# Performance work log

Measured on AMD Instinct MI355X. Metric: run time of the kernel, lower is better.

The kernel has to match this reference:

```python
import jax, jax.numpy as jnp
import numpy as np

jax.config.update("jax_enable_x64", True)  # hash math needs int64 (prime * coord > 2^31)

LEVEL = 16
MOD_T = 2 ** 16
FDIM = 3
_PRIMES = (1, 2654435761, 805459861)  # first feature_dim primes from the module


def _grid_sizes():
    # mirrors torch float32 computation: b = exp((log(n_max)-log(n_min))/(level-1))
    n_min = np.float32(4.0)
    n_max = np.float32(256.0)
    b = np.float32(np.exp((np.log(n_max) - np.log(n_min)) / np.float32(LEVEL - 1)))
    return [int(n_min * b ** i) for i in range(LEVEL)]


def setup_inputs() -> dict:
    key = jax.random.key(0)
    k1, k2 = jax.random.split(key)
    images = jax.random.uniform(k1, (16, 3, 256, 256), dtype=jnp.float32)
    hash_table = (jax.random.uniform(k2, (LEVEL, MOD_T, FDIM), dtype=jnp.float32)
                  * 0.0002 - 0.0001)
    return {"images": images, "hash_table": hash_table}


def reference(images, hash_table):
    b, c, h, w = images.shape
    primes = jnp.array(_PRIMES[:FDIM], dtype=jnp.int64)
    neg_inf = jnp.array(-jnp.inf, dtype=images.dtype)
    outs = []
    for lvl, grid in enumerate(_grid_sizes()):
        kh, kw = h // grid, w // grid
        # max_pool2d(images*grid, kernel=(kh,kw), stride=(kh,kw))
        pooled = jax.lax.reduce_window(
            images * grid, neg_inf, jax.lax.max,
            window_dimensions=(1, 1, kh, kw),
            window_strides=(1, 1, kh, kw),
            padding="VALID")                     # [B, F, gh, gw]
        idx = pooled.astype(jnp.int64) * primes[None, :, None, None]
        g = idx[:, 0]
        for i in range(1, FDIM):
            g = g ^ idx[:, i]
        g = g % MOD_T                             # [B, gh, gw]
        f = hash_table[lvl][g]                    # gather -> [B, gh, gw, F]
        f = jnp.transpose(f, (0, 3, 1, 2))        # [B, F, gh, gw]
        # F.interpolate(..., mode='bilinear') == half-pixel, align_corners=False
        f = jax.image.resize(f, (b, FDIM, h, w), method="bilinear")
        outs.append(f)
    return jnp.concatenate(outs, axis=1)          # [B, level*F, H, W]
```

## Files before the change

### kernel.cpp

```cpp
#include <hip/hip_runtime.h>
#include <stdint.h>
#include <math.h>


#define NLVL 16
#define NB   16

__constant__ int   c_P[NLVL]   = {4,5,6,9,12,15,21,28,36,51,64,85,128,256,256,256};
__constant__ float c_G[NLVL]   = {4.f,5.f,6.f,9.f,12.f,15.f,21.f,27.f,36.f,48.f,63.f,84.f,111.f,147.f,194.f,255.f};
__constant__ int   c_CUM[14]   = {0,16,41,77,158,302,527,968,1752,3048,5649,9745,16970,33354};

#define CELLS_PB   33354
#define CELLS_TOT  (CELLS_PB*NB)
#define MWS_FLOATS (CELLS_TOT*3)
#define POOL_BLOCKS (NB*32)
#define DIR_BLOCKS  1024
#define TILE_BLOCKS (13*16*16)
#define K2_BLOCKS   (DIR_BLOCKS + TILE_BLOCKS)

__device__ __forceinline__ uint32_t hash3(float m0, float m1, float m2, float g) {
    uint32_t v0 = (uint32_t)(int)(m0 * g);
    uint32_t v1 = (uint32_t)(int)(m1 * g);
    uint32_t v2 = (uint32_t)(int)(m2 * g);
    return (v0 ^ (v1 * 2654435761u) ^ (v2 * 805459861u)) & 0xFFFFu;
}

__global__ __launch_bounds__(256) void pool_single(const float* __restrict__ img,
                                                   unsigned int* __restrict__ mws)
{
    static constexpr int K_P[13]   = {4,5,6,9,12,15,21,28,36,51,64,85,128};
    static constexpr int K_KH[13]  = {64,51,42,28,21,17,12,9,7,5,4,3,2};
    static constexpr int K_CUM[13] = {0,16,41,77,158,302,527,968,1752,3048,5649,9745,16970};

    __shared__ float simg[3][8][256];
    __shared__ float colbuf[3][256];

    int b    = blockIdx.x >> 5;
    int band = blockIdx.x & 31;
    int y0   = band * 8;

    const float* base = img + (size_t)b * 196608 + (size_t)y0 * 256;
    for (int t = threadIdx.x; t < 1536; t += 256) {
        int ch = t >> 9;
        int r  = t & 511;
        float4 v = *(const float4*)(base + (size_t)ch * 65536 + r * 4);
        int row = r >> 6, c4 = (r & 63) << 2;
        simg[ch][row][c4 + 0] = v.x;
        simg[ch][row][c4 + 1] = v.y;
        simg[ch][row][c4 + 2] = v.z;
        simg[ch][row][c4 + 3] = v.w;
    }
    __syncthreads();

    int x = threadIdx.x;
#pragma unroll
    for (int lvl = 0; lvl < 13; ++lvl) {
        const int kh = K_KH[lvl], P = K_P[lvl];
        int nr0 = y0 / kh;
        int nr1 = (y0 + 7) / kh; if (nr1 > P - 1) nr1 = P - 1;
        for (int cr = nr0; cr <= nr1; ++cr) {
            int rlo = cr * kh;      if (rlo < y0) rlo = y0;
            int rhi = cr * kh + kh; if (rhi > y0 + 8) rhi = y0 + 8;
            float p0 = -INFINITY, p1 = -INFINITY, p2 = -INFINITY;
            for (int r = rlo; r < rhi; ++r) {
                int rr = r - y0;
                p0 = fmaxf(p0, simg[0][rr][x]);
                p1 = fmaxf(p1, simg[1][rr][x]);
                p2 = fmaxf(p2, simg[2][rr][x]);
            }
            colbuf[0][x] = p0; colbuf[1][x] = p1; colbuf[2][x] = p2;
            __syncthreads();
            if (x < P) {
                float q0 = -INFINITY, q1 = -INFINITY, q2 = -INFINITY;
                for (int c = x * kh; c < x * kh + kh; ++c) {
                    q0 = fmaxf(q0, colbuf[0][c]);
                    q1 = fmaxf(q1, colbuf[1][c]);
                    q2 = fmaxf(q2, colbuf[2][c]);
                }
                int idx = K_CUM[lvl] * NB + b * P * P + cr * P + x;
                atomicMax(&mws[idx],                 __float_as_uint(q0));
                atomicMax(&mws[idx + CELLS_TOT],     __float_as_uint(q1));
                atomicMax(&mws[idx + 2 * CELLS_TOT], __float_as_uint(q2));
            }
            __syncthreads();
        }
    }
}

__global__ __launch_bounds__(256) void render(const float* __restrict__ img,
                                              const float* __restrict__ tab,
                                              const float* __restrict__ mws,
                                              float* __restrict__ out)
{
    __shared__ float4 s[34 * 34];
    if (blockIdx.x < DIR_BLOCKS) {
        int t = blockIdx.x * 256 + threadIdx.x;
        int b = t >> 14;
        int pix0 = (t & 16383) << 2;
        const float* p = img + (size_t)b * 196608 + pix0;
        float4 i0 = *(const float4*)p;
        float4 i1 = *(const float4*)(p + 65536);
        float4 i2 = *(const float4*)(p + 131072);
#pragma unroll
        for (int lvl = 13; lvl < 16; ++lvl) {
            float g = c_G[lvl];
            const float* T = tab + (size_t)lvl * 196608;
            uint32_t g0 = hash3(i0.x, i1.x, i2.x, g);
            uint32_t g1 = hash3(i0.y, i1.y, i2.y, g);
            uint32_t g2 = hash3(i0.z, i1.z, i2.z, g);
            uint32_t g3 = hash3(i0.w, i1.w, i2.w, g);
            float3 f0 = *(const float3*)(T + g0 * 3);
            float3 f1 = *(const float3*)(T + g1 * 3);
            float3 f2 = *(const float3*)(T + g2 * 3);
            float3 f3 = *(const float3*)(T + g3 * 3);
            float4 o0, o1, o2;
            o0.x = f0.x; o1.x = f0.y; o2.x = f0.z;
            o0.y = f1.x; o1.y = f1.y; o2.y = f1.z;
            o0.z = f2.x; o1.z = f2.y; o2.z = f2.z;
            o0.w = f3.x; o1.w = f3.y; o2.w = f3.z;
            float* ob = out + ((size_t)b * 48 + 3 * lvl) * 65536 + pix0;
            *(float4*)ob            = o0;
            *(float4*)(ob + 65536)  = o1;
            *(float4*)(ob + 131072) = o2;
        }
        return;
    }

    int blk   = blockIdx.x - DIR_BLOCKS;
    int tile  = blk & 15;
    int plane = blk >> 4;
    int lvl   = plane >> 4;
    int b     = plane & 15;
    int P     = c_P[lvl];
    int yt0   = (tile >> 2) * 64;
    int xt0   = (tile & 3) * 64;

    int nlo  = ((2 * yt0 + 1) * P - 256) >> 9;
    int r_lo = nlo < 0 ? 0 : (nlo > P - 1 ? P - 1 : nlo);
    int nhi  = (((2 * (yt0 + 63) + 1) * P - 256) >> 9) + 1;
    int r_hi = nhi < 0 ? 0 : (nhi > P - 1 ? P - 1 : nhi);
    int mlo  = ((2 * xt0 + 1) * P - 256) >> 9;
    int c_lo = mlo < 0 ? 0 : (mlo > P - 1 ? P - 1 : mlo);
    int mhi  = (((2 * (xt0 + 63) + 1) * P - 256) >> 9) + 1;
    int c_hi = mhi < 0 ? 0 : (mhi > P - 1 ? P - 1 : mhi);
    int span_y = r_hi - r_lo + 1;
    int span_x = c_hi - c_lo + 1;

    int planebase = c_CUM[lvl] * NB + b * P * P;
    const float* T = tab + (size_t)lvl * 196608;
    float gmul = c_G[lvl];
    int n = span_y * span_x;
    for (int t = threadIdx.x; t < n; t += 256) {
        int r = t / span_x, c = t - r * span_x;
        int idx = planebase + (r_lo + r) * P + c_lo + c;
        float m0 = mws[idx];
        float m1 = mws[idx + CELLS_TOT];
        float m2 = mws[idx + 2 * CELLS_TOT];
        uint32_t g = hash3(m0, m1, m2, gmul);
        float3 tv = *(const float3*)(T + g * 3);
        float4 fv; fv.x = tv.x; fv.y = tv.y; fv.z = tv.z; fv.w = 0.f;
        s[t] = fv;
    }
    __syncthreads();

    int lane = threadIdx.x & 63;
    int w    = threadIdx.x >> 6;
    int xq   = lane & 15;
    int rg   = lane >> 4;
    int xb   = xt0 + xq * 4;

    int ix0t[4], ix1t[4]; float wx1t[4];
#pragma unroll
    for (int j = 0; j < 4; ++j) {
        int numx = (2 * (xb + j) + 1) * P - 256;
        int ix0  = numx >> 9;
        float fx = (float)(numx & 511) * (1.0f / 512.0f);
        int ix1;
        if (ix0 < 0)           { ix0 = 0;     ix1 = 0;     fx = 0.f; }
        else if (ix0 >= P - 1) { ix0 = P - 1; ix1 = P - 1; fx = 0.f; }
        else                   { ix1 = ix0 + 1; }
        ix0t[j] = ix0 - c_lo; ix1t[j] = ix1 - c_lo; wx1t[j] = fx;
    }

#pragma unroll
    for (int k = 0; k < 4; ++k) {
        int y = yt0 + w * 16 + rg * 4 + k;
        int numy = (2 * y + 1) * P - 256;
        int iy0  = numy >> 9;
        float fy = (float)(numy & 511) * (1.0f / 512.0f);
        int iy1;
        if (iy0 < 0)           { iy0 = 0;     iy1 = 0;     fy = 0.f; }
        else if (iy0 >= P - 1) { iy0 = P - 1; iy1 = P - 1; fy = 0.f; }
        else                   { iy1 = iy0 + 1; }
        const float4* p0 = s + (iy0 - r_lo) * span_x;
        const float4* p1 = s + (iy1 - r_lo) * span_x;
        float wy1 = fy, wy0 = 1.f - fy;

        float v[3][4];
#pragma unroll
        for (int j = 0; j < 4; ++j) {
            float wx1 = wx1t[j], wx0 = 1.f - wx1;
            float4 t00 = p0[ix0t[j]];
            float4 t01 = p0[ix1t[j]];
            float4 t10 = p1[ix0t[j]];
            float4 t11 = p1[ix1t[j]];
            v[0][j] = wy0 * (wx0 * t00.x + wx1 * t01.x) + wy1 * (wx0 * t10.x + wx1 * t11.x);
            v[1][j] = wy0 * (wx0 * t00.y + wx1 * t01.y) + wy1 * (wx0 * t10.y + wx1 * t11.y);
            v[2][j] = wy0 * (wx0 * t00.z + wx1 * t01.z) + wy1 * (wx0 * t10.z + wx1 * t11.z);
        }
        float* o = out + ((size_t)b * 48 + 3 * lvl) * 65536 + (size_t)y * 256 + xb;
#pragma unroll
        for (int c = 0; c < 3; ++c) {
            float4 q; q.x = v[c][0]; q.y = v[c][1]; q.z = v[c][2]; q.w = v[c][3];
            *(float4*)(o + (size_t)c * 65536) = q;
        }
    }
}

extern "C" void kernel_launch(void* const* d_in, const int* in_sizes, int n_in,
                              void* d_out, int out_size, void* d_ws, size_t ws_size,
                              hipStream_t stream)
{
    const float* img = (const float*)d_in[0];
    const float* tab = (const float*)d_in[1];
    float* out = (float*)d_out;
    float* mws = (float*)d_ws;

    hipMemsetAsync(mws, 0, (size_t)MWS_FLOATS * sizeof(float), stream);
    hipLaunchKernelGGL(pool_single, dim3(POOL_BLOCKS), dim3(256), 0, stream, img, (unsigned int*)mws);
    hipLaunchKernelGGL(render,      dim3(K2_BLOCKS), dim3(256), 0, stream, img, tab, mws, out);
}
```

Before: 82.49 us.

## Restructure pooling into 4-row bands, use nontemporal stores and row-reuse interpolation

Pooling now runs on 4-row bands with twice as many blocks. It precomputes a 4-row column max and assigns one (cell row, cell column) per thread, which removes the per-row __syncthreads. For levels whose kernel height is 2 or 4 it uses plain stores instead of atomics. The render kernel switches to one column per lane and walks 16 rows, reusing horizontally interpolated source rows across output rows, and all output writes become nontemporal stores. The aim is less sync and atomic overhead, fewer LDS reads, and avoiding cache pollution on the write-bound output. The cost is scalar per-lane stores instead of float4 and possible divergence in the pooling loops.

```diff
diff --git a/kernel.cpp b/kernel.cpp
--- a/kernel.cpp
+++ b/kernel.cpp
@@ -6,6 +6,8 @@
 #define NLVL 16
 #define NB   16
 
+typedef float nvec4 __attribute__((ext_vector_type(4)));
+
 __constant__ int   c_P[NLVL]   = {4,5,6,9,12,15,21,28,36,51,64,85,128,256,256,256};
 __constant__ float c_G[NLVL]   = {4.f,5.f,6.f,9.f,12.f,15.f,21.f,27.f,36.f,48.f,63.f,84.f,111.f,147.f,194.f,255.f};
 __constant__ int   c_CUM[14]   = {0,16,41,77,158,302,527,968,1752,3048,5649,9745,16970,33354};
@@ -13,7 +15,7 @@
 #define CELLS_PB   33354
 #define CELLS_TOT  (CELLS_PB*NB)
 #define MWS_FLOATS (CELLS_TOT*3)
-#define POOL_BLOCKS (NB*32)
+#define POOL_BLOCKS (NB*64)
 #define DIR_BLOCKS  1024
 #define TILE_BLOCKS (13*16*16)
 #define K2_BLOCKS   (DIR_BLOCKS + TILE_BLOCKS)
@@ -23,6 +25,11 @@
     uint32_t v1 = (uint32_t)(int)(m1 * g);
     uint32_t v2 = (uint32_t)(int)(m2 * g);
     return (v0 ^ (v1 * 2654435761u) ^ (v2 * 805459861u)) & 0xFFFFu;
+}
+
+__device__ __forceinline__ void nt_store4(float* p, float a, float b, float c, float d) {
+    nvec4 v; v.x = a; v.y = b; v.z = c; v.w = d;
+    __builtin_nontemporal_store(v, (nvec4*)p);
 }
 
 __global__ __launch_bounds__(256) void pool_single(const float* __restrict__ img,
@@ -32,19 +39,20 @@
     static constexpr int K_KH[13]  = {64,51,42,28,21,17,12,9,7,5,4,3,2};
     static constexpr int K_CUM[13] = {0,16,41,77,158,302,527,968,1752,3048,5649,9745,16970};
 
-    __shared__ float simg[3][8][256];
-    __shared__ float colbuf[3][256];
-
-    int b    = blockIdx.x >> 5;
-    int band = blockIdx.x & 31;
-    int y0   = band * 8;
+    __shared__ float simg[3][4][256];
+    __shared__ float cmax[3][256];
+
+    int b    = blockIdx.x >> 6;
+    int band = blockIdx.x & 63;
+    int y0   = band * 4;
 
     const float* base = img + (size_t)b * 196608 + (size_t)y0 * 256;
-    for (int t = threadIdx.x; t < 1536; t += 256) {
-        int ch = t >> 9;
-        int r  = t & 511;
-        float4 v = *(const float4*)(base + (size_t)ch * 65536 + r * 4);
-        int row = r >> 6, c4 = (r & 63) << 2;
+    for (int t = threadIdx.x; t < 768; t += 256) {
+        int ch  = t >> 8;
+        int rem = t & 255;
+        int row = rem >> 6, cg = rem & 63;
+        float4 v = *(const float4*)(base + (size_t)ch * 65536 + row * 256 + cg * 4);
+        int c4 = cg << 2;
         simg[ch][row][c4 + 0] = v.x;
         simg[ch][row][c4 + 1] = v.y;
         simg[ch][row][c4 + 2] = v.z;
@@ -52,37 +60,55 @@
     }
     __syncthreads();
 
-    int x = threadIdx.x;
+    {
+        int x = threadIdx.x;
+#pragma unroll
+        for (int ch = 0; ch < 3; ++ch)
+            cmax[ch][x] = fmaxf(fmaxf(simg[ch][0][x], simg[ch][1][x]),
+                                fmaxf(simg[ch][2][x], simg[ch][3][x]));
+    }
+    __syncthreads();
+
 #pragma unroll
     for (int lvl = 0; lvl < 13; ++lvl) {
         const int kh = K_KH[lvl], P = K_P[lvl];
         int nr0 = y0 / kh;
-        int nr1 = (y0 + 7) / kh; if (nr1 > P - 1) nr1 = P - 1;
-        for (int cr = nr0; cr <= nr1; ++cr) {
+        int nr1 = (y0 + 3) / kh; if (nr1 > P - 1) nr1 = P - 1;
+        int cnt = (nr1 - nr0 + 1) * P;
+        for (int t = threadIdx.x; t < cnt; t += 256) {
+            int dcr = t / P;
+            int cx  = t - dcr * P;
+            int cr  = nr0 + dcr;
             int rlo = cr * kh;      if (rlo < y0) rlo = y0;
-            int rhi = cr * kh + kh; if (rhi > y0 + 8) rhi = y0 + 8;
-            float p0 = -INFINITY, p1 = -INFINITY, p2 = -INFINITY;
-            for (int r = rlo; r < rhi; ++r) {
-                int rr = r - y0;
-                p0 = fmaxf(p0, simg[0][rr][x]);
-                p1 = fmaxf(p1, simg[1][rr][x]);
-                p2 = fmaxf(p2, simg[2][rr][x]);
+            int rhi = cr * kh + kh; if (rhi > y0 + 4) rhi = y0 + 4;
+            int cA = cx * kh, cB = cA + kh;
+            float m0 = -INFINITY, m1 = -INFINITY, m2 = -INFINITY;
+            if (rlo == y0 && rhi == y0 + 4) {
+                for (int c = cA; c < cB; ++c) {
+                    m0 = fmaxf(m0, cmax[0][c]);
+                    m1 = fmaxf(m1, cmax[1][c]);
+                    m2 = fmaxf(m2, cmax[2][c]);
+                }
+            } else {
+                for (int r = rlo; r < rhi; ++r) {
+                    int rr = r - y0;
+                    for (int c = cA; c < cB; ++c) {
+                        m0 = fmaxf(m0, simg[0][rr][c]);
+                        m1 = fmaxf(m1, simg[1][rr][c]);
+                        m2 = fmaxf(m2, simg[2][rr][c]);
+                    }
+                }
             }
-            colbuf[0][x] = p0; colbuf[1][x] = p1; colbuf[2][x] = p2;
-            __syncthreads();
-            if (x < P) {
-                float q0 = -INFINITY, q1 = -INFINITY, q2 = -INFINITY;
-                for (int c = x * kh; c < x * kh + kh; ++c) {
-                    q0 = fmaxf(q0, colbuf[0][c]);
-                    q1 = fmaxf(q1, colbuf[1][c]);
-                    q2 = fmaxf(q2, colbuf[2][c]);
-                }
-                int idx = K_CUM[lvl] * NB + b * P * P + cr * P + x;
-                atomicMax(&mws[idx],                 __float_as_uint(q0));
-                atomicMax(&mws[idx + CELLS_TOT],     __float_as_uint(q1));
-                atomicMax(&mws[idx + 2 * CELLS_TOT], __float_as_uint(q2));
+            int idx = K_CUM[lvl] * NB + b * P * P + cr * P + cx;
+            if (kh == 2 || kh == 4) {
+                mws[idx]                 = __float_as_uint(m0);
+                mws[idx + CELLS_TOT]     = __float_as_uint(m1);
+                mws[idx + 2 * CELLS_TOT] = __float_as_uint(m2);
+            } else {
+                atomicMax(&mws[idx],                 __float_as_uint(m0));
+                atomicMax(&mws[idx + CELLS_TOT],     __float_as_uint(m1));
+                atomicMax(&mws[idx + 2 * CELLS_TOT], __float_as_uint(m2));
             }
-            __syncthreads();
         }
     }
 }
@@ -113,15 +139,10 @@
             float3 f1 = *(const float3*)(T + g1 * 3);
             float3 f2 = *(const float3*)(T + g2 * 3);
             float3 f3 = *(const float3*)(T + g3 * 3);
-            float4 o0, o1, o2;
-            o0.x = f0.x; o1.x = f0.y; o2.x = f0.z;
-            o0.y = f1.x; o1.y = f1.y; o2.y = f1.z;
-            o0.z = f2.x; o1.z = f2.y; o2.z = f2.z;
-            o0.w = f3.x; o1.w = f3.y; o2.w = f3.z;
             float* ob = out + ((size_t)b * 48 + 3 * lvl) * 65536 + pix0;
-            *(float4*)ob            = o0;
-            *(float4*)(ob + 65536)  = o1;
-            *(float4*)(ob + 131072) = o2;
+            nt_store4(ob,            f0.x, f1.x, f2.x, f3.x);
+            nt_store4(ob + 65536,    f0.y, f1.y, f2.y, f3.y);
+            nt_store4(ob + 131072,   f0.z, f1.z, f2.z, f3.z);
         }
         return;
     }
@@ -165,26 +186,25 @@
 
     int lane = threadIdx.x & 63;
     int w    = threadIdx.x >> 6;
-    int xq   = lane & 15;
-    int rg   = lane >> 4;
-    int xb   = xt0 + xq * 4;
-
-    int ix0t[4], ix1t[4]; float wx1t[4];
-#pragma unroll
-    for (int j = 0; j < 4; ++j) {
-        int numx = (2 * (xb + j) + 1) * P - 256;
-        int ix0  = numx >> 9;
-        float fx = (float)(numx & 511) * (1.0f / 512.0f);
-        int ix1;
-        if (ix0 < 0)           { ix0 = 0;     ix1 = 0;     fx = 0.f; }
-        else if (ix0 >= P - 1) { ix0 = P - 1; ix1 = P - 1; fx = 0.f; }
-        else                   { ix1 = ix0 + 1; }
-        ix0t[j] = ix0 - c_lo; ix1t[j] = ix1 - c_lo; wx1t[j] = fx;
-    }
-
-#pragma unroll
-    for (int k = 0; k < 4; ++k) {
-        int y = yt0 + w * 16 + rg * 4 + k;
+    int x    = xt0 + lane;
+
+    int numx = (2 * x + 1) * P - 256;
+    int ix0  = numx >> 9;
+    float fx = (float)(numx & 511) * (1.0f / 512.0f);
+    int ix1;
+    if (ix0 < 0)           { ix0 = 0;     ix1 = 0;     fx = 0.f; }
+    else if (ix0 >= P - 1) { ix0 = P - 1; ix1 = P - 1; fx = 0.f; }
+    else                   { ix1 = ix0 + 1; }
+    int cA = ix0 - c_lo, cB = ix1 - c_lo;
+    float wx0 = 1.f - fx, wx1 = fx;
+
+    int cur0 = -1, cur1 = -1;
+    float r0x = 0.f, r0y = 0.f, r0z = 0.f;
+    float r1x = 0.f, r1y = 0.f, r1z = 0.f;
+    float* obase = out + ((size_t)b * 48 + 3 * lvl) * 65536 + x;
+
+    for (int k = 0; k < 16; ++k) {
+        int y = yt0 + w * 16 + k;
         int numy = (2 * y + 1) * P - 256;
         int iy0  = numy >> 9;
         float fy = (float)(numy & 511) * (1.0f / 512.0f);
@@ -192,28 +212,32 @@
         if (iy0 < 0)           { iy0 = 0;     iy1 = 0;     fy = 0.f; }
         else if (iy0 >= P - 1) { iy0 = P - 1; iy1 = P - 1; fy = 0.f; }
         else                   { iy1 = iy0 + 1; }
-        const float4* p0 = s + (iy0 - r_lo) * span_x;
-        const float4* p1 = s + (iy1 - r_lo) * span_x;
-        float wy1 = fy, wy0 = 1.f - fy;
-
-        float v[3][4];
-#pragma unroll
-        for (int j = 0; j < 4; ++j) {
-            float wx1 = wx1t[j], wx0 = 1.f - wx1;
-            float4 t00 = p0[ix0t[j]];
-            float4 t01 = p0[ix1t[j]];
-            float4 t10 = p1[ix0t[j]];
-            float4 t11 = p1[ix1t[j]];
-            v[0][j] = wy0 * (wx0 * t00.x + wx1 * t01.x) + wy1 * (wx0 * t10.x + wx1 * t11.x);
-            v[1][j] = wy0 * (wx0 * t00.y + wx1 * t01.y) + wy1 * (wx0 * t10.y + wx1 * t11.y);
-            v[2][j] = wy0 * (wx0 * t00.z + wx1 * t01.z) + wy1 * (wx0 * t10.z + wx1 * t11.z);
-        }
-        float* o = out + ((size_t)b * 48 + 3 * lvl) * 65536 + (size_t)y * 256 + xb;
-#pragma unroll
-        for (int c = 0; c < 3; ++c) {
-            float4 q; q.x = v[c][0]; q.y = v[c][1]; q.z = v[c][2]; q.w = v[c][3];
-            *(float4*)(o + (size_t)c * 65536) = q;
-        }
+
+        if (iy0 != cur0) {
+            if (iy0 == cur1) { r0x = r1x; r0y = r1y; r0z = r1z; }
+            else {
+                const float4* p = s + (iy0 - r_lo) * span_x;
+                float4 a = p[cA], q = p[cB];
+                r0x = wx0 * a.x + wx1 * q.x;
+                r0y = wx0 * a.y + wx1 * q.y;
+                r0z = wx0 * a.z + wx1 * q.z;
+            }
+            cur0 = iy0;
+        }
+        if (iy1 != cur1) {
+            const float4* p = s + (iy1 - r_lo) * span_x;
+            float4 a = p[cA], q = p[cB];
+            r1x = wx0 * a.x + wx1 * q.x;
+            r1y = wx0 * a.y + wx1 * q.y;
+            r1z = wx0 * a.z + wx1 * q.z;
+            cur1 = iy1;
+        }
+
+        float wy0 = 1.f - fy, wy1 = fy;
+        float* o = obase + (size_t)y * 256;
+        __builtin_nontemporal_store(wy0 * r0x + wy1 * r1x, o);
+        __builtin_nontemporal_store(wy0 * r0y + wy1 * r1y, o + 65536);
+        __builtin_nontemporal_store(wy0 * r0z + wy1 * r1z, o + 131072);
     }
 }
 
@@ -226,7 +250,7 @@
     float* out = (float*)d_out;
     float* mws = (float*)d_ws;
 
-    hipMemsetAsync(mws, 0, (size_t)MWS_FLOATS * sizeof(float), stream);
+    (void)hipMemsetAsync(mws, 0, (size_t)MWS_FLOATS * sizeof(float), stream);
     hipLaunchKernelGGL(pool_single, dim3(POOL_BLOCKS), dim3(256), 0, stream, img, (unsigned int*)mws);
     hipLaunchKernelGGL(render,      dim3(K2_BLOCKS), dim3(256), 0, stream, img, tab, mws, out);
 }
```

After: 89.73 us. +8.8%, slower.
